# Kernel tuning notes

Measured on AMD Instinct MI355X. Metric: run time of the kernel, lower is better.

## Reference

```python
import jax, jax.numpy as jnp
import numpy as np

WIDTH_IN = 8
WIDTH_OUT = 8
STRIDES = (1, 1)
PADDING = 'SAME'


def quantizer(x, width, mode='round', clip=True):
    """Fixed-point quantization to `width` bits in [-1, 1), straight-through estimator.

    mode='round' -> round-to-nearest; mode='floor' -> truncate.
    clip=True saturates to the representable range [-1, 1 - 2^-(width-1)].
    """
    scale = jnp.asarray(2.0 ** (width - 1), x.dtype)
    q = jnp.round(x * scale) if mode == 'round' else jnp.floor(x * scale)
    q = q / scale
    # straight-through: forward uses q, gradient flows as identity
    q = x + jax.lax.stop_gradient(q - x)
    if clip:
        q = jnp.clip(q, -1.0, 1.0 - 1.0 / scale)
    return q


def setup_inputs() -> dict:
    key = jax.random.key(0)
    kx, kw = jax.random.split(key)
    x = jax.random.normal(kx, (32, 112, 112, 64), dtype=jnp.float32)      # NHWC
    kernels = jax.random.normal(kw, (3, 3, 64, 128), dtype=jnp.float32) * 0.05  # HWIO, RandomNormal init
    return {"x": x, "kernels": kernels}


def reference(x, kernels):
    # Method == 'Fixed' path of MyConv2D.call
    xq = quantizer(x, WIDTH_IN, 'round', clip=True)                # quantize activations
    kq = quantizer(kernels, WIDTH_IN, 'round', clip=True)          # quantize weights
    out = jax.lax.conv_general_dilated(
        xq, kq,
        window_strides=STRIDES,
        padding=PADDING,
        dimension_numbers=('NHWC', 'HWIO', 'NHWC'),
    )                                                              # [B, 112, 112, 128]
    out = quantizer(out, WIDTH_OUT, 'floor', clip=False)           # quantize output, truncating
    return out
```

## Files before the change

### kernel.cpp

```cpp
#include <hip/hip_runtime.h>

#define NIMG 32
#define H 112
#define W 112
#define CI 64
#define CO 128
#define GP2 56

typedef __attribute__((ext_vector_type(8))) __bf16 bf16x8;
typedef __attribute__((ext_vector_type(4))) float f32x4;
typedef __attribute__((ext_vector_type(4))) short short4v;
typedef __attribute__((ext_vector_type(4))) int int4v;

__device__ __forceinline__ short q8bits(float v) {
    float t = rintf(v * 128.0f);
    t = fminf(fmaxf(t, -128.0f), 127.0f);
    union { float f; unsigned u; } cv; cv.f = t;
    return (short)(cv.u >> 16);
}
__device__ __forceinline__ int q8i(float v) {
    float t = rintf(v * 128.0f);
    t = fminf(fmaxf(t, -128.0f), 127.0f);
    return (int)t;
}

__global__ __launch_bounds__(256) void quant_pack_w_i8(const float* __restrict__ w,
                                                       signed char* __restrict__ bp) {
    int idx = blockIdx.x * 256 + threadIdx.x;
    int j  = idx & 15;
    int l  = (idx >> 4) & 63;
    int nt = (idx >> 10) & 7;
    int kk = idx >> 13;
    int k = kk * 64 + (l >> 4) * 16 + j;
    int n = nt * 16 + (l & 15);
    bp[idx] = (signed char)q8i(w[k * CO + n]);
}

#define RB 7296

__global__ __launch_bounds__(256) void conv_i8f(const float* __restrict__ x,
                                                const signed char* __restrict__ bp,
                                                float* __restrict__ out) {
    __shared__ __align__(16) signed char xs[4 * RB];
    int bid0 = blockIdx.x;
    int bid = (bid0 & 7) * 224 + (bid0 >> 3);
    int n = bid / GP2;
    int g = bid - n * GP2;
    int h0 = g * 2;
    int tid  = threadIdx.x;
    int lane = tid & 63;
    int wave = tid >> 6;

    if (tid < 32)
        *(int4v*)&xs[(tid >> 3) * RB + ((tid & 4) ? 113 : 0) * 64 + (tid & 3) * 16] =
            (int4v){0, 0, 0, 0};

    #pragma unroll
    for (int r = 0; r < 4; ++r) {
        int hr = h0 - 1 + r;
        signed char* dst = &xs[r * RB + 64];
        if ((unsigned)hr < (unsigned)H) {
            const float* src = x + ((size_t)(n * H + hr) * W) * CI;
            float4 v[7];
            #pragma unroll
            for (int k = 0; k < 7; ++k) v[k] = *(const float4*)&src[k * 1024 + tid * 4];
            #pragma unroll
            for (int k = 0; k < 7; ++k) {
                int b = (q8i(v[k].x) & 255) | ((q8i(v[k].y) & 255) << 8) |
                        ((q8i(v[k].z) & 255) << 16) | (q8i(v[k].w) << 24);
                *(int*)&dst[k * 1024 + tid * 4] = b;
            }
        } else {
            #pragma unroll
            for (int k = 0; k < 7; ++k)
                *(int*)&dst[k * 1024 + tid * 4] = 0;
        }
    }
    __syncthreads();

    int lane15 = lane & 15;
    int hi     = lane >> 4;
    int nt0    = wave * 2;
    const int4v* bp4 = (const int4v*)bp;

    #pragma unroll
    for (int trow = 0; trow < 2; ++trow) {
        int4v acc[7][2];
        #pragma unroll
        for (int mt = 0; mt < 7; ++mt) {
            acc[mt][0] = (int4v){0, 0, 0, 0};
            acc[mt][1] = (int4v){0, 0, 0, 0};
        }

        #pragma unroll
        for (int r = 0; r < 3; ++r) {
            int sbase = (trow + r) * RB;
            #pragma unroll
            for (int s = 0; s < 3; ++s) {
                int kk = r * 3 + s;
                int4v b0 = bp4[(kk * 8 + nt0    ) * 64 + lane];
                int4v b1 = bp4[(kk * 8 + nt0 + 1) * 64 + lane];
                int abase = sbase + (s + lane15) * 64 + hi * 16;
                #pragma unroll
                for (int mt = 0; mt < 7; ++mt) {
                    int4v a = *(const int4v*)&xs[abase + mt * 1024];
                    acc[mt][0] = __builtin_amdgcn_mfma_i32_16x16x64_i8(a, b0, acc[mt][0], 0, 0, 0);
                    acc[mt][1] = __builtin_amdgcn_mfma_i32_16x16x64_i8(a, b1, acc[mt][1], 0, 0, 0);
                }
            }
        }

        float* orow = out + (size_t)((n * H + h0 + trow) * W) * CO;
        int co0  = wave * 32 + lane15;
        int rowb = hi * 4;
        #pragma unroll
        for (int mt = 0; mt < 7; ++mt)
            #pragma unroll
            for (int t = 0; t < 2; ++t)
                #pragma unroll
                for (int rg = 0; rg < 4; ++rg) {
                    int m = mt * 16 + rowb + rg;
                    orow[m * CO + co0 + t * 16] =
                        (float)(acc[mt][t][rg] >> 7) * 0.0078125f;
                }
    }
}

__global__ __launch_bounds__(256) void quant_pack_w(const float* __restrict__ w,
                                                    short* __restrict__ bp) {
    int idx = blockIdx.x * 256 + threadIdx.x;
    int j    = idx & 7;
    int lane = (idx >> 3) & 63;
    int nt   = (idx >> 9) & 7;
    int kt   = idx >> 12;
    int k = kt * 32 + (lane >> 4) * 8 + j;
    int n = nt * 16 + (lane & 15);
    bp[idx] = q8bits(w[k * CO + n]);
}

#define LDSW 114
#define LDST 72
__global__ __launch_bounds__(256) void conv_fb(const float* __restrict__ x,
                                               const short* __restrict__ bp,
                                               float* __restrict__ out) {
    __shared__ short xs[3 * LDSW * LDST];
    int bid = blockIdx.x;
    int n = bid / H;
    int h = bid - n * H;
    int tid = threadIdx.x;
    const float* xin = x + (size_t)n * (H * W * CI);
    for (int r = 0; r < 3; ++r) {
        int hrow = h + r - 1;
        bool rowok = ((unsigned)hrow < (unsigned)H);
        const float* srow = xin + (size_t)hrow * (W * CI);
        for (int t = tid; t < LDSW * 16; t += 256) {
            int c = t >> 4;
            int ci4 = (t & 15) << 2;
            int wcol = c - 1;
            float4 v = {0.f, 0.f, 0.f, 0.f};
            if (rowok && (unsigned)wcol < (unsigned)W)
                v = *(const float4*)&srow[wcol * CI + ci4];
            short4v sv;
            sv.x = q8bits(v.x); sv.y = q8bits(v.y);
            sv.z = q8bits(v.z); sv.w = q8bits(v.w);
            *(short4v*)&xs[(r * LDSW + c) * LDST + ci4] = sv;
        }
    }
    __syncthreads();
    int lane = tid & 63;
    int wave = tid >> 6;
    int laneoff = (lane & 15) * LDST + (lane >> 4) * 8;
    const bf16x8* bfr = (const bf16x8*)bp;
    int nt0 = wave * 2;
    f32x4 acc[7][2];
    #pragma unroll
    for (int mt = 0; mt < 7; ++mt) {
        acc[mt][0] = (f32x4){0.f, 0.f, 0.f, 0.f};
        acc[mt][1] = (f32x4){0.f, 0.f, 0.f, 0.f};
    }
    #pragma unroll
    for (int kk = 0; kk < 18; ++kk) {
        int rs = kk >> 1;
        int r = rs / 3;
        int s = rs - r * 3;
        bf16x8 b0 = bfr[(kk * 8 + nt0    ) * 64 + lane];
        bf16x8 b1 = bfr[(kk * 8 + nt0 + 1) * 64 + lane];
        int abase = (r * LDSW + s) * LDST + (kk & 1) * 32 + laneoff;
        #pragma unroll
        for (int mt = 0; mt < 7; ++mt) {
            bf16x8 a = *(const bf16x8*)&xs[abase + mt * 16 * LDST];
            acc[mt][0] = __builtin_amdgcn_mfma_f32_16x16x32_bf16(a, b0, acc[mt][0], 0, 0, 0);
            acc[mt][1] = __builtin_amdgcn_mfma_f32_16x16x32_bf16(a, b1, acc[mt][1], 0, 0, 0);
        }
    }
    float* orow = out + (size_t)(n * H + h) * (W * CO);
    int colc = wave * 32 + (lane & 15);
    int rowb = (lane >> 4) * 4;
    #pragma unroll
    for (int mt = 0; mt < 7; ++mt)
        #pragma unroll
        for (int t2 = 0; t2 < 2; ++t2)
            #pragma unroll
            for (int rg = 0; rg < 4; ++rg) {
                int m = mt * 16 + rowb + rg;
                orow[m * CO + colc + t2 * 16] =
                    floorf(acc[mt][t2][rg] * 0.0078125f) * 0.0078125f;
            }
}

extern "C" void kernel_launch(void* const* d_in, const int* in_sizes, int n_in,
                              void* d_out, int out_size, void* d_ws, size_t ws_size,
                              hipStream_t stream) {
    const float* x = (const float*)d_in[0];
    const float* w = (const float*)d_in[1];
    float* out = (float*)d_out;

    const size_t BPI8_BYTES = 73728;

    if (ws_size >= BPI8_BYTES) {
        signed char* bp8 = (signed char*)d_ws;
        quant_pack_w_i8<<<288, 256, 0, stream>>>(w, bp8);
        conv_i8f<<<NIMG * GP2, 256, 0, stream>>>(x, bp8, out);
    } else {
        short* bp = (short*)d_ws;
        quant_pack_w<<<288, 256, 0, stream>>>(w, bp);
        conv_fb<<<NIMG * H, 256, 0, stream>>>(x, bp, out);
    }
}
```

Before: 305.4 us.

## Pre-quantize input into padded int8 buffer and read conv operands from global

Adds a separate pass that quantizes the float input once into a zero-padded int8 NHWC workspace. The conv kernel then drops its LDS staging and barrier, handles one output row per block, and loads MFMA A operands straight from global/L2. This removes the redundant re-quantization of halo rows across blocks and the LDS round trip. In exchange it adds an extra kernel launch, writes and rereads a ~26MB int8 tensor, and needs a larger workspace; otherwise it falls back to the bf16 path.

```diff
diff --git a/kernel.cpp b/kernel.cpp
--- a/kernel.cpp
+++ b/kernel.cpp
@@ -5,7 +5,7 @@
 #define W 112
 #define CI 64
 #define CO 128
-#define GP2 56
+#define HP 114
 
 typedef __attribute__((ext_vector_type(8))) __bf16 bf16x8;
 typedef __attribute__((ext_vector_type(4))) float f32x4;
@@ -24,8 +24,8 @@
     return (int)t;
 }
 
-__global__ __launch_bounds__(256) void quant_pack_w_i8(const float* __restrict__ w,
-                                                       signed char* __restrict__ bp) {
+__global__ __launch_bounds__(256) void prep_pack(const float* __restrict__ w,
+                                                 signed char* __restrict__ bp) {
     int idx = blockIdx.x * 256 + threadIdx.x;
     int j  = idx & 15;
     int l  = (idx >> 4) & 63;
@@ -36,94 +36,88 @@
     bp[idx] = (signed char)q8i(w[k * CO + n]);
 }
 
-#define RB 7296
-
-__global__ __launch_bounds__(256) void conv_i8f(const float* __restrict__ x,
+__global__ __launch_bounds__(256) void prep_x(const float* __restrict__ x,
+                                              signed char* __restrict__ xqp) {
+    int p   = blockIdx.x;
+    int tid = threadIdx.x;
+    int n  = p / HP;
+    int hp = p - n * HP;
+    size_t rb = ((size_t)(n * HP + hp)) * (HP * 64);
+    if (hp == 0 || hp == HP - 1) {
+        for (int t = tid; t < 456; t += 256)
+            *(int4v*)&xqp[rb + (size_t)t * 16] = (int4v){0, 0, 0, 0};
+        return;
+    }
+    if (tid < 8) {
+        int c = (tid & 4) ? (HP - 1) : 0;
+        *(int4v*)&xqp[rb + c * 64 + (tid & 3) * 16] = (int4v){0, 0, 0, 0};
+    }
+    const float* src = x + ((size_t)(n * H + hp - 1) * W) * CI;
+    #pragma unroll
+    for (int k = 0; k < 7; ++k) {
+        float4 v = *(const float4*)&src[k * 1024 + tid * 4];
+        int b = (q8i(v.x) & 255) | ((q8i(v.y) & 255) << 8) |
+                ((q8i(v.z) & 255) << 16) | (q8i(v.w) << 24);
+        int L = k * 1024 + tid * 4;
+        *(int*)&xqp[rb + 64 + L] = b;
+    }
+}
+
+__global__ __launch_bounds__(256) void conv_dir(const signed char* __restrict__ xqp,
                                                 const signed char* __restrict__ bp,
                                                 float* __restrict__ out) {
-    __shared__ __align__(16) signed char xs[4 * RB];
     int bid0 = blockIdx.x;
-    int bid = (bid0 & 7) * 224 + (bid0 >> 3);
-    int n = bid / GP2;
-    int g = bid - n * GP2;
-    int h0 = g * 2;
+    int bid = (bid0 & 7) * 448 + (bid0 >> 3);
+    int n = bid / H;
+    int h = bid - n * H;
     int tid  = threadIdx.x;
     int lane = tid & 63;
     int wave = tid >> 6;
-
-    if (tid < 32)
-        *(int4v*)&xs[(tid >> 3) * RB + ((tid & 4) ? 113 : 0) * 64 + (tid & 3) * 16] =
-            (int4v){0, 0, 0, 0};
-
-    #pragma unroll
-    for (int r = 0; r < 4; ++r) {
-        int hr = h0 - 1 + r;
-        signed char* dst = &xs[r * RB + 64];
-        if ((unsigned)hr < (unsigned)H) {
-            const float* src = x + ((size_t)(n * H + hr) * W) * CI;
-            float4 v[7];
-            #pragma unroll
-            for (int k = 0; k < 7; ++k) v[k] = *(const float4*)&src[k * 1024 + tid * 4];
-            #pragma unroll
-            for (int k = 0; k < 7; ++k) {
-                int b = (q8i(v[k].x) & 255) | ((q8i(v[k].y) & 255) << 8) |
-                        ((q8i(v[k].z) & 255) << 16) | (q8i(v[k].w) << 24);
-                *(int*)&dst[k * 1024 + tid * 4] = b;
-            }
-        } else {
-            #pragma unroll
-            for (int k = 0; k < 7; ++k)
-                *(int*)&dst[k * 1024 + tid * 4] = 0;
-        }
-    }
-    __syncthreads();
-
     int lane15 = lane & 15;
     int hi     = lane >> 4;
     int nt0    = wave * 2;
     const int4v* bp4 = (const int4v*)bp;
 
-    #pragma unroll
-    for (int trow = 0; trow < 2; ++trow) {
-        int4v acc[7][2];
-        #pragma unroll
-        for (int mt = 0; mt < 7; ++mt) {
-            acc[mt][0] = (int4v){0, 0, 0, 0};
-            acc[mt][1] = (int4v){0, 0, 0, 0};
-        }
-
-        #pragma unroll
-        for (int r = 0; r < 3; ++r) {
-            int sbase = (trow + r) * RB;
+    const signed char* ab0 =
+        xqp + (((size_t)(n * HP + h)) * HP + lane15) * 64 + hi * 16;
+
+    int4v acc[7][2];
+    #pragma unroll
+    for (int mt = 0; mt < 7; ++mt) {
+        acc[mt][0] = (int4v){0, 0, 0, 0};
+        acc[mt][1] = (int4v){0, 0, 0, 0};
+    }
+
+    #pragma unroll
+    for (int r = 0; r < 3; ++r) {
+        #pragma unroll
+        for (int s = 0; s < 3; ++s) {
+            int kk = r * 3 + s;
+            int4v b0 = bp4[(kk * 8 + nt0    ) * 64 + lane];
+            int4v b1 = bp4[(kk * 8 + nt0 + 1) * 64 + lane];
+            const signed char* ab = ab0 + (r * HP + s) * 64;
             #pragma unroll
-            for (int s = 0; s < 3; ++s) {
-                int kk = r * 3 + s;
-                int4v b0 = bp4[(kk * 8 + nt0    ) * 64 + lane];
-                int4v b1 = bp4[(kk * 8 + nt0 + 1) * 64 + lane];
-                int abase = sbase + (s + lane15) * 64 + hi * 16;
-                #pragma unroll
-                for (int mt = 0; mt < 7; ++mt) {
-                    int4v a = *(const int4v*)&xs[abase + mt * 1024];
-                    acc[mt][0] = __builtin_amdgcn_mfma_i32_16x16x64_i8(a, b0, acc[mt][0], 0, 0, 0);
-                    acc[mt][1] = __builtin_amdgcn_mfma_i32_16x16x64_i8(a, b1, acc[mt][1], 0, 0, 0);
-                }
+            for (int mt = 0; mt < 7; ++mt) {
+                int4v a = *(const int4v*)(ab + mt * 1024);
+                acc[mt][0] = __builtin_amdgcn_mfma_i32_16x16x64_i8(a, b0, acc[mt][0], 0, 0, 0);
+                acc[mt][1] = __builtin_amdgcn_mfma_i32_16x16x64_i8(a, b1, acc[mt][1], 0, 0, 0);
             }
         }
-
-        float* orow = out + (size_t)((n * H + h0 + trow) * W) * CO;
-        int co0  = wave * 32 + lane15;
-        int rowb = hi * 4;
-        #pragma unroll
-        for (int mt = 0; mt < 7; ++mt)
+    }
+
+    float* orow = out + (size_t)((n * H + h) * W) * CO;
+    int co0  = wave * 32 + lane15;
+    int rowb = hi * 4;
+    #pragma unroll
+    for (int mt = 0; mt < 7; ++mt)
+        #pragma unroll
+        for (int t = 0; t < 2; ++t)
             #pragma unroll
-            for (int t = 0; t < 2; ++t)
-                #pragma unroll
-                for (int rg = 0; rg < 4; ++rg) {
-                    int m = mt * 16 + rowb + rg;
-                    orow[m * CO + co0 + t * 16] =
-                        (float)(acc[mt][t][rg] >> 7) * 0.0078125f;
-                }
-    }
+            for (int rg = 0; rg < 4; ++rg) {
+                int m = mt * 16 + rowb + rg;
+                orow[m * CO + co0 + t * 16] =
+                    (float)(acc[mt][t][rg] >> 7) * 0.0078125f;
+            }
 }
 
 __global__ __launch_bounds__(256) void quant_pack_w(const float* __restrict__ w,
@@ -216,11 +210,14 @@
     float* out = (float*)d_out;
 
     const size_t BPI8_BYTES = 73728;
-
-    if (ws_size >= BPI8_BYTES) {
+    const size_t XQP_BYTES  = (size_t)NIMG * HP * HP * CI;
+
+    if (ws_size >= BPI8_BYTES + XQP_BYTES) {
         signed char* bp8 = (signed char*)d_ws;
-        quant_pack_w_i8<<<288, 256, 0, stream>>>(w, bp8);
-        conv_i8f<<<NIMG * GP2, 256, 0, stream>>>(x, bp8, out);
+        signed char* xqp = (signed char*)d_ws + BPI8_BYTES;
+        prep_pack<<<288, 256, 0, stream>>>(w, bp8);
+        prep_x<<<NIMG * HP, 256, 0, stream>>>(x, xqp);
+        conv_dir<<<NIMG * H, 256, 0, stream>>>(xqp, bp8, out);
     } else {
         short* bp = (short*)d_ws;
         quant_pack_w<<<288, 256, 0, stream>>>(w, bp);
```

Result: slower. 335.4 us (+9.8%).
